# Optimization experiments

Hardware: AMD Instinct MI355X
Metric: run time of the kernel (lower is better)

## Reference

```python
import jax, jax.numpy as jnp
from jax import lax
import numpy as np

H, W = 240, 304
IN_CH, OUT_CH, K = 16, 32, 3
B = 8
N_PER = 65536
N = B * N_PER
CIN = IN_CH + 2  # pos + neg + features


def setup_inputs() -> dict:
    key = jax.random.key(0)
    k1, k2, k3, k4, k5 = jax.random.split(key, 5)
    # events columns: x, y, t in [0,1); polarity in {0,1}
    xyt = jax.random.uniform(k1, (N, 3), dtype=jnp.float32)
    pol = jax.random.randint(k2, (N, 1), 0, 2).astype(jnp.float32)
    events = jnp.concatenate([xyt, pol], axis=1)
    features = jax.random.normal(k3, (N, IN_CH), dtype=jnp.float32)
    offsets = (jnp.arange(1, B + 1, dtype=jnp.int64) * N_PER)  # cumulative counts
    # SubmanifoldConvolution params: one [CIN, OUT_CH] matrix per filter offset -> HWIO
    fan_in = K * K * CIN
    weight = jax.random.normal(k4, (K, K, CIN, OUT_CH), dtype=jnp.float32) / np.sqrt(fan_in)
    bias = jax.random.normal(k5, (OUT_CH,), dtype=jnp.float32) * 0.01
    return {"events": events, "features": features, "weight": weight,
            "bias": bias, "offsets": offsets}


def reference(events, features, weight, bias, offsets):
    n = events.shape[0]
    b = offsets.shape[0]
    # offset2batch: row i belongs to first sample whose cumulative offset exceeds i
    batch = jnp.searchsorted(offsets, jnp.arange(n, dtype=offsets.dtype), side="right").astype(jnp.int32)
    pos = events[:, 3:4]
    neg = 1.0 - pos
    sparse = jnp.concatenate([pos, neg, features], axis=1)  # [N, CIN]
    # yx = events[:, [1, 0]] scaled by (h, w), rounded to grid coords
    yi = jnp.clip(jnp.round(events[:, 1] * H).astype(jnp.int32), 0, H - 1)
    xi = jnp.clip(jnp.round(events[:, 0] * W).astype(jnp.int32), 0, W - 1)
    key = (batch * H + yi) * W + xi  # linear site id, [N]
    nseg = b * H * W
    # scn InputLayer mode=4: average features of duplicate coordinates
    feat_sum = jax.ops.segment_sum(sparse, key, num_segments=nseg)  # [nseg, CIN]
    cnt = jax.ops.segment_sum(jnp.ones((n,), sparse.dtype), key, num_segments=nseg)
    dense = feat_sum / jnp.maximum(cnt, 1.0)[:, None]
    dense = dense.reshape(b, H, W, CIN)  # zeros at inactive sites
    # Submanifold 3x3 conv: inactive neighbors are zero, so a dense SAME conv
    # evaluated only at active sites matches the submanifold rulebook math.
    out = lax.conv_general_dilated(dense, weight, window_strides=(1, 1),
                                   padding="SAME",
                                   dimension_numbers=("NHWC", "HWIO", "NHWC"))
    out = out.reshape(nseg, OUT_CH)
    # OutputLayer: read back per input row (active sites only), add bias there
    f = out[key] + bias  # [N, OUT_CH]
    return f
```

## Files before the change

### kernel.cpp

```cpp
#include <hip/hip_runtime.h>

#define Hh 240
#define Ww 304
#define IN_CH 16
#define OUT_CH 32
#define Bb 8
#define N_PER 65536
#define N_EV (Bb * N_PER)
#define CIN (IN_CH + 2)
#define NSEG (Bb * Hh * Ww)
#define NBLK 570

#define TW 32
#define TH 8
#define HW_ 34
#define HH_ 10
#define HALO_PIX (HH_ * HW_)
#define NXT_TILES 10
#define NYT_TILES 30
#define OPITCH 33

typedef __attribute__((ext_vector_type(8))) short bf16x8;
typedef __attribute__((ext_vector_type(4))) float f32x4;

__device__ __forceinline__ unsigned short f2bf(float x) {
  unsigned u = __float_as_uint(x);
  unsigned r = u + 0x7fffu + ((u >> 16) & 1u);
  return (unsigned short)(r >> 16);
}
__device__ __forceinline__ float bf2f(unsigned short b) {
  return __uint_as_float(((unsigned)b) << 16);
}
__device__ __forceinline__ unsigned pk2(float a, float b) {
  return (unsigned)f2bf(a) | ((unsigned)f2bf(b) << 16);
}

__global__ __launch_bounds__(256) void hist_rank_kernel(
    const float* __restrict__ events, const int* __restrict__ offsets,
    int* __restrict__ hist, int2* __restrict__ kr) {
  int i = blockIdx.x * blockDim.x + threadIdx.x;
  float4 ev = ((const float4*)events)[i];
  int yi = (int)rintf(ev.y * (float)Hh);
  yi = min(max(yi, 0), Hh - 1);
  int xi = (int)rintf(ev.x * (float)Ww);
  xi = min(max(xi, 0), Ww - 1);
  int b = 0;
#pragma unroll
  for (int j = 0; j < Bb; j++) b += (offsets[j] <= i) ? 1 : 0;
  int key = (b * Hh + yi) * Ww + xi;
  int pol = (ev.w != 0.0f) ? 1 : 0;
  int rank = atomicAdd(&hist[key], 1);
  kr[i] = make_int2(key | (pol << 31), rank);
}

__global__ __launch_bounds__(256) void scan1_kernel(
    const int* __restrict__ hist, int* __restrict__ baseLocal,
    int* __restrict__ blockSum) {
  __shared__ int lds[256];
  int b = blockIdx.x, t = threadIdx.x;
  int idx = b * 1024 + t * 4;
  int4 v = *(const int4*)(hist + idx);
  int s0 = v.x, s1 = s0 + v.y, s2 = s1 + v.z, s3 = s2 + v.w;
  lds[t] = s3;
  __syncthreads();
  int val = s3;
  for (int off = 1; off < 256; off <<= 1) {
    int n = (t >= off) ? lds[t - off] : 0;
    __syncthreads();
    val += n;
    lds[t] = val;
    __syncthreads();
  }
  int excl = val - s3;
  int4 o;
  o.x = excl; o.y = excl + s0; o.z = excl + s1; o.w = excl + s2;
  *(int4*)(baseLocal + idx) = o;
  if (t == 255) blockSum[b] = val;
}

__global__ __launch_bounds__(1024) void scan2_weights_kernel(
    const int* __restrict__ blockSum, int* __restrict__ blockOffset,
    const float* __restrict__ weight, unsigned short* __restrict__ wprep) {
  int t = threadIdx.x;
  if (blockIdx.x == 1) {
#pragma unroll
    for (int it = 0; it < 6; it++) {
      int idx = it * 1024 + t;
      int ky = idx >> 11;
      int rem = idx & 2047;
      int n = rem >> 6;
      int kl = rem & 63;
      unsigned short v = 0;
      if (kl < 54) {
        int kx = kl / 18, ci = kl - kx * 18;
        v = f2bf(weight[((ky * 3 + kx) * CIN + ci) * OUT_CH + n]);
      }
      wprep[idx] = v;
    }
    return;
  }
  __shared__ int lds[1024];
  int v = (t < NBLK) ? blockSum[t] : 0;
  lds[t] = v;
  __syncthreads();
  int val = v;
  for (int off = 1; off < 1024; off <<= 1) {
    int n = (t >= off) ? lds[t - off] : 0;
    __syncthreads();
    val += n;
    lds[t] = val;
    __syncthreads();
  }
  if (t < NBLK) blockOffset[t] = val - v;
  if (t == 0) blockOffset[NBLK] = lds[1023];
}

__global__ __launch_bounds__(256) void scatter_rec_kernel(
    const float* __restrict__ features, const int2* __restrict__ kr,
    const int* __restrict__ baseLocal, const int* __restrict__ blockOffset,
    uint4* __restrict__ sortedRec, int* __restrict__ sortedMeta) {
  int i = blockIdx.x * blockDim.x + threadIdx.x;
  int2 m = kr[i];
  int key = m.x & 0x7fffffff;
  int pos = baseLocal[key] + blockOffset[key >> 10] + m.y;
  const float4* f = (const float4*)(features + (size_t)i * IN_CH);
  float4 f0 = f[0], f1 = f[1], f2 = f[2], f3 = f[3];
  unsigned meta = (unsigned)i | ((unsigned)m.x & 0x80000000u);
  uint4* R = sortedRec + (size_t)pos * 3;
  R[0] = make_uint4(meta, pk2(f0.x, f0.y), pk2(f0.z, f0.w), pk2(f1.x, f1.y));
  R[1] = make_uint4(pk2(f1.z, f1.w), pk2(f2.x, f2.y), pk2(f2.z, f2.w),
                    pk2(f3.x, f3.y));
  R[2] = make_uint4(pk2(f3.z, f3.w), 0, 0, 0);
  sortedMeta[pos] = (int)meta;
}

__device__ __forceinline__ void accum_pixel(unsigned* smem,
                                            const uint4* __restrict__ sortedRec,
                                            int h, int base, int c) {
  float acc[CIN];
#pragma unroll
  for (int k = 0; k < CIN; k++) acc[k] = 0.0f;
  for (int j = 0; j < c; j++) {
    const uint4* R = sortedRec + (size_t)(base + j) * 3;
    uint4 r0 = R[0], r1 = R[1];
    unsigned d8 = ((const unsigned*)R)[8];
    float pol = (float)(r0.x >> 31);
    acc[0] += pol;
    acc[1] += 1.0f - pol;
    acc[2]  += bf2f((unsigned short)r0.y);  acc[3]  += bf2f((unsigned short)(r0.y >> 16));
    acc[4]  += bf2f((unsigned short)r0.z);  acc[5]  += bf2f((unsigned short)(r0.z >> 16));
    acc[6]  += bf2f((unsigned short)r0.w);  acc[7]  += bf2f((unsigned short)(r0.w >> 16));
    acc[8]  += bf2f((unsigned short)r1.x);  acc[9]  += bf2f((unsigned short)(r1.x >> 16));
    acc[10] += bf2f((unsigned short)r1.y);  acc[11] += bf2f((unsigned short)(r1.y >> 16));
    acc[12] += bf2f((unsigned short)r1.z);  acc[13] += bf2f((unsigned short)(r1.z >> 16));
    acc[14] += bf2f((unsigned short)r1.w);  acc[15] += bf2f((unsigned short)(r1.w >> 16));
    acc[16] += bf2f((unsigned short)d8);    acc[17] += bf2f((unsigned short)(d8 >> 16));
  }
  float inv = 1.0f / fmaxf((float)c, 1.0f);
  unsigned* row = smem + 9 * h;
#pragma unroll
  for (int k = 0; k < 9; k++) row[k] = pk2(acc[2 * k] * inv, acc[2 * k + 1] * inv);
}

__global__ __launch_bounds__(256) void fused_conv_kernel(
    const uint4* __restrict__ sortedRec, const int* __restrict__ sortedMeta,
    const int* __restrict__ baseLocal, const int* __restrict__ blockOffset,
    const unsigned short* __restrict__ wprep, const float* __restrict__ bias,
    float* __restrict__ out) {
  __shared__ unsigned smem[128 * OPITCH];
  __shared__ int ibase[TH * TW];
  __shared__ int icnt[TH * TW];

  int blk = blockIdx.x;
  int xt = blk % NXT_TILES;
  int rem = blk / NXT_TILES;
  int yt = rem % NYT_TILES;
  int b = rem / NYT_TILES;
  int x0 = xt * TW, y0 = yt * TH;
  int tid = threadIdx.x;

  if (tid < 12) smem[3060 + tid] = 0;

  int hA = tid, hB = tid + 256;
  bool hasB = hB < HALO_PIX;
  int baseA = 0, cA = 0, baseB = 0, cB = 0;
  {
    int hy = hA / HW_, hx = hA % HW_;
    int gy = y0 - 1 + hy, gx = x0 - 1 + hx;
    if (gy >= 0 && gy < Hh && gx >= 0 && gx < Ww) {
      int p = (b * Hh + gy) * Ww + gx;
      int bo = blockOffset[p >> 10];
      baseA = baseLocal[p] + bo;
      int nxt = ((p & 1023) != 1023) ? (baseLocal[p + 1] + bo)
                                     : blockOffset[(p >> 10) + 1];
      cA = nxt - baseA;
    }
  }
  if (hasB) {
    int hy = hB / HW_, hx = hB % HW_;
    int gy = y0 - 1 + hy, gx = x0 - 1 + hx;
    if (gy >= 0 && gy < Hh && gx >= 0 && gx < Ww) {
      int p = (b * Hh + gy) * Ww + gx;
      int bo = blockOffset[p >> 10];
      baseB = baseLocal[p] + bo;
      int nxt = ((p & 1023) != 1023) ? (baseLocal[p + 1] + bo)
                                     : blockOffset[(p >> 10) + 1];
      cB = nxt - baseB;
    }
  }
  accum_pixel(smem, sortedRec, hA, baseA, cA);
  if (hasB) accum_pixel(smem, sortedRec, hB, baseB, cB);
  {
    int hy = hA / HW_, hx = hA % HW_;
    if (hx >= 1 && hx <= TW && hy >= 1 && hy <= TH) {
      int t = (hy - 1) * TW + (hx - 1);
      ibase[t] = baseA;
      icnt[t] = cA;
    }
  }
  if (hasB) {
    int hy = hB / HW_, hx = hB % HW_;
    if (hx >= 1 && hx <= TW && hy >= 1 && hy <= TH) {
      int t = (hy - 1) * TW + (hx - 1);
      ibase[t] = baseB;
      icnt[t] = cB;
    }
  }
  __syncthreads();

  int wv = tid >> 6, lane = tid & 63;
  int quad = lane >> 4, lrow = lane & 15;

  f32x4 accf[4][2];
#pragma unroll
  for (int i = 0; i < 4; i++)
#pragma unroll
    for (int nt = 0; nt < 2; nt++) accf[i][nt] = (f32x4){0.f, 0.f, 0.f, 0.f};

  const unsigned* hp = smem;
#pragma unroll
  for (int ky = 0; ky < 3; ky++) {
    bf16x8 bfr[2][2];
#pragma unroll
    for (int kh = 0; kh < 2; kh++)
#pragma unroll
      for (int nt = 0; nt < 2; nt++) {
        int n = nt * 16 + lrow;
        bfr[kh][nt] = *(const bf16x8*)(wprep + ((ky * 32 + n) << 6) +
                                       kh * 32 + quad * 8);
      }
#pragma unroll
    for (int i = 0; i < 4; i++) {
      int t0 = (wv * 4 + i) * 16;
      int ox = (t0 & 31) + lrow;
      int oy = t0 >> 5;
      int idx0 = ((oy + ky) * HW_ + ox) * CIN;
#pragma unroll
      for (int kh = 0; kh < 2; kh++) {
        union { bf16x8 v; unsigned u[4]; } a;
        int ui = (idx0 >> 1) + kh * 16 + quad * 4;
        a.u[0] = hp[ui]; a.u[1] = hp[ui + 1];
        a.u[2] = hp[ui + 2]; a.u[3] = hp[ui + 3];
        accf[i][0] = __builtin_amdgcn_mfma_f32_16x16x32_bf16(
            a.v, bfr[kh][0], accf[i][0], 0, 0, 0);
        accf[i][1] = __builtin_amdgcn_mfma_f32_16x16x32_bf16(
            a.v, bfr[kh][1], accf[i][1], 0, 0, 0);
      }
    }
  }
  __syncthreads();

  float* outsh = (float*)smem;
  float bn0 = bias[lrow], bn1 = bias[16 + lrow];
  int gx = x0 + (tid & 31);
  int c = icnt[tid];
  int base = ibase[tid];
#pragma unroll
  for (int ch = 0; ch < 2; ch++) {
#pragma unroll
    for (int ii = 0; ii < 2; ii++) {
      int i = ch * 2 + ii;
      int lidx = ii * 16 + quad * 4;
      int row = wv * 32 + lidx;
#pragma unroll
      for (int r = 0; r < 4; r++) {
        outsh[(row + r) * OPITCH + lrow] = accf[i][0][r] + bn0;
        outsh[(row + r) * OPITCH + 16 + lrow] = accf[i][1][r] + bn1;
      }
    }
    __syncthreads();
    if (((tid >> 5) & 1) == ch && gx < Ww && c > 0) {
      int row = (tid >> 6) * 32 + ((tid & 63) - ch * 32);
      const float* rp = outsh + row * OPITCH;
      float4 o0 = make_float4(rp[0], rp[1], rp[2], rp[3]);
      float4 o1 = make_float4(rp[4], rp[5], rp[6], rp[7]);
      float4 o2 = make_float4(rp[8], rp[9], rp[10], rp[11]);
      float4 o3 = make_float4(rp[12], rp[13], rp[14], rp[15]);
      float4 o4 = make_float4(rp[16], rp[17], rp[18], rp[19]);
      float4 o5 = make_float4(rp[20], rp[21], rp[22], rp[23]);
      float4 o6 = make_float4(rp[24], rp[25], rp[26], rp[27]);
      float4 o7 = make_float4(rp[28], rp[29], rp[30], rp[31]);
      for (int j = 0; j < c; j++) {
        int ev = sortedMeta[base + j] & 0x7fffffff;
        float4* op = (float4*)(out + (size_t)ev * OUT_CH);
        op[0] = o0; op[1] = o1; op[2] = o2; op[3] = o3;
        op[4] = o4; op[5] = o5; op[6] = o6; op[7] = o7;
      }
    }
    __syncthreads();
  }
}

extern "C" void kernel_launch(void* const* d_in, const int* in_sizes, int n_in,
                              void* d_out, int out_size, void* d_ws,
                              size_t ws_size, hipStream_t stream) {
  const float* events = (const float*)d_in[0];
  const float* features = (const float*)d_in[1];
  const float* weight = (const float*)d_in[2];
  const float* bias = (const float*)d_in[3];
  const int* offsets = (const int*)d_in[4];
  float* out = (float*)d_out;

  uint4* sortedRec = (uint4*)d_ws;
  int* sortedMeta = (int*)(sortedRec + (size_t)N_EV * 3);
  int2* kr = (int2*)(sortedMeta + N_EV);
  int* hist = (int*)(kr + N_EV);
  int* baseLocal = hist + NSEG;
  int* blockOffset = baseLocal + NSEG;
  int* blockSum = blockOffset + 1024;
  unsigned short* wprep = (unsigned short*)(blockSum + 1024);

  hipMemsetAsync(hist, 0, (size_t)NSEG * sizeof(int), stream);

  hist_rank_kernel<<<N_EV / 256, 256, 0, stream>>>(events, offsets, hist, kr);
  scan1_kernel<<<NBLK, 256, 0, stream>>>(hist, baseLocal, blockSum);
  scan2_weights_kernel<<<2, 1024, 0, stream>>>(blockSum, blockOffset, weight,
                                               wprep);
  scatter_rec_kernel<<<N_EV / 256, 256, 0, stream>>>(
      features, kr, baseLocal, blockOffset, sortedRec, sortedMeta);
  fused_conv_kernel<<<Bb * NYT_TILES * NXT_TILES, 256, 0, stream>>>(
      sortedRec, sortedMeta, baseLocal, blockOffset, wprep, bias, out);
}
```

Baseline: 194.9 us.

## Split per-pixel averaging into separate densify kernel with padded dense grid

Per-pixel averaging of duplicate events moves out of the conv kernel into a new densify kernel. It writes a padded bf16 dense grid (10 dwords per pixel), which the conv kernel loads as a halo tile. This stops each conv block from recomputing the halo pixels it shares with neighbouring tiles. Polarity is now stored as pre-packed bf16 in 64-byte records, the scan runs in place, and the weight layout is repadded to a 20-channel stride. The cost is an extra launch plus a write and read of the full dense grid, which is roughly 23 MB.

```diff
diff --git a/kernel.cpp b/kernel.cpp
--- a/kernel.cpp
+++ b/kernel.cpp
@@ -11,14 +11,17 @@
 #define NSEG (Bb * Hh * Ww)
 #define NBLK 570
 
+#define DP 10
+
 #define TW 32
 #define TH 8
 #define HW_ 34
 #define HH_ 10
-#define HALO_PIX (HH_ * HW_)
 #define NXT_TILES 10
 #define NYT_TILES 30
 #define OPITCH 33
+#define HALO_DW (HH_ * HW_ * DP)
+#define HALO_LD 3424
 
 typedef __attribute__((ext_vector_type(8))) short bf16x8;
 typedef __attribute__((ext_vector_type(4))) float f32x4;
@@ -53,13 +56,12 @@
   kr[i] = make_int2(key | (pol << 31), rank);
 }
 
-__global__ __launch_bounds__(256) void scan1_kernel(
-    const int* __restrict__ hist, int* __restrict__ baseLocal,
-    int* __restrict__ blockSum) {
+__global__ __launch_bounds__(256) void scan1_kernel(int* __restrict__ data,
+                                                    int* __restrict__ blockSum) {
   __shared__ int lds[256];
   int b = blockIdx.x, t = threadIdx.x;
   int idx = b * 1024 + t * 4;
-  int4 v = *(const int4*)(hist + idx);
+  int4 v = *(const int4*)(data + idx);
   int s0 = v.x, s1 = s0 + v.y, s2 = s1 + v.z, s3 = s2 + v.w;
   lds[t] = s3;
   __syncthreads();
@@ -74,7 +76,7 @@
   int excl = val - s3;
   int4 o;
   o.x = excl; o.y = excl + s0; o.z = excl + s1; o.w = excl + s2;
-  *(int4*)(baseLocal + idx) = o;
+  *(int4*)(data + idx) = o;
   if (t == 255) blockSum[b] = val;
 }
 
@@ -91,9 +93,9 @@
       int n = rem >> 6;
       int kl = rem & 63;
       unsigned short v = 0;
-      if (kl < 54) {
-        int kx = kl / 18, ci = kl - kx * 18;
-        v = f2bf(weight[((ky * 3 + kx) * CIN + ci) * OUT_CH + n]);
+      if (kl < 60) {
+        int kx = kl / 20, ci = kl - kx * 20;
+        if (ci < 18) v = f2bf(weight[((ky * 3 + kx) * CIN + ci) * OUT_CH + n]);
       }
       wprep[idx] = v;
     }
@@ -123,30 +125,36 @@
   int2 m = kr[i];
   int key = m.x & 0x7fffffff;
   int pos = baseLocal[key] + blockOffset[key >> 10] + m.y;
+  float pol = (float)(((unsigned)m.x) >> 31);
   const float4* f = (const float4*)(features + (size_t)i * IN_CH);
   float4 f0 = f[0], f1 = f[1], f2 = f[2], f3 = f[3];
-  unsigned meta = (unsigned)i | ((unsigned)m.x & 0x80000000u);
-  uint4* R = sortedRec + (size_t)pos * 3;
-  R[0] = make_uint4(meta, pk2(f0.x, f0.y), pk2(f0.z, f0.w), pk2(f1.x, f1.y));
+  uint4* R = sortedRec + (size_t)pos * 4;
+  R[0] = make_uint4(pk2(pol, 1.0f - pol), pk2(f0.x, f0.y), pk2(f0.z, f0.w),
+                    pk2(f1.x, f1.y));
   R[1] = make_uint4(pk2(f1.z, f1.w), pk2(f2.x, f2.y), pk2(f2.z, f2.w),
                     pk2(f3.x, f3.y));
   R[2] = make_uint4(pk2(f3.z, f3.w), 0, 0, 0);
-  sortedMeta[pos] = (int)meta;
-}
-
-__device__ __forceinline__ void accum_pixel(unsigned* smem,
-                                            const uint4* __restrict__ sortedRec,
-                                            int h, int base, int c) {
+  R[3] = make_uint4(0, 0, 0, 0);
+  sortedMeta[pos] = i;
+}
+
+__global__ __launch_bounds__(256) void densify_kernel(
+    const uint4* __restrict__ sortedRec, const int* __restrict__ baseLocal,
+    const int* __restrict__ blockOffset, unsigned* __restrict__ dense) {
+  int p = blockIdx.x * 256 + threadIdx.x;
+  int bo = blockOffset[p >> 10];
+  int base = baseLocal[p] + bo;
+  int nxt = ((p & 1023) != 1023) ? (baseLocal[p + 1] + bo)
+                                 : blockOffset[(p >> 10) + 1];
+  int c = nxt - base;
   float acc[CIN];
 #pragma unroll
   for (int k = 0; k < CIN; k++) acc[k] = 0.0f;
   for (int j = 0; j < c; j++) {
-    const uint4* R = sortedRec + (size_t)(base + j) * 3;
+    const uint4* R = sortedRec + (size_t)(base + j) * 4;
     uint4 r0 = R[0], r1 = R[1];
     unsigned d8 = ((const unsigned*)R)[8];
-    float pol = (float)(r0.x >> 31);
-    acc[0] += pol;
-    acc[1] += 1.0f - pol;
+    acc[0]  += bf2f((unsigned short)r0.x);  acc[1]  += bf2f((unsigned short)(r0.x >> 16));
     acc[2]  += bf2f((unsigned short)r0.y);  acc[3]  += bf2f((unsigned short)(r0.y >> 16));
     acc[4]  += bf2f((unsigned short)r0.z);  acc[5]  += bf2f((unsigned short)(r0.z >> 16));
     acc[6]  += bf2f((unsigned short)r0.w);  acc[7]  += bf2f((unsigned short)(r0.w >> 16));
@@ -157,19 +165,18 @@
     acc[16] += bf2f((unsigned short)d8);    acc[17] += bf2f((unsigned short)(d8 >> 16));
   }
   float inv = 1.0f / fmaxf((float)c, 1.0f);
-  unsigned* row = smem + 9 * h;
-#pragma unroll
-  for (int k = 0; k < 9; k++) row[k] = pk2(acc[2 * k] * inv, acc[2 * k + 1] * inv);
+  unsigned* dp = dense + (size_t)p * DP;
+#pragma unroll
+  for (int k = 0; k < 9; k++) dp[k] = pk2(acc[2 * k] * inv, acc[2 * k + 1] * inv);
+  dp[9] = 0;
 }
 
 __global__ __launch_bounds__(256) void fused_conv_kernel(
-    const uint4* __restrict__ sortedRec, const int* __restrict__ sortedMeta,
+    const unsigned* __restrict__ dense, const int* __restrict__ sortedMeta,
     const int* __restrict__ baseLocal, const int* __restrict__ blockOffset,
     const unsigned short* __restrict__ wprep, const float* __restrict__ bias,
     float* __restrict__ out) {
   __shared__ unsigned smem[128 * OPITCH];
-  __shared__ int ibase[TH * TW];
-  __shared__ int icnt[TH * TW];
 
   int blk = blockIdx.x;
   int xt = blk % NXT_TILES;
@@ -179,52 +186,29 @@
   int x0 = xt * TW, y0 = yt * TH;
   int tid = threadIdx.x;
 
-  if (tid < 12) smem[3060 + tid] = 0;
-
-  int hA = tid, hB = tid + 256;
-  bool hasB = hB < HALO_PIX;
-  int baseA = 0, cA = 0, baseB = 0, cB = 0;
-  {
-    int hy = hA / HW_, hx = hA % HW_;
-    int gy = y0 - 1 + hy, gx = x0 - 1 + hx;
-    if (gy >= 0 && gy < Hh && gx >= 0 && gx < Ww) {
-      int p = (b * Hh + gy) * Ww + gx;
-      int bo = blockOffset[p >> 10];
-      baseA = baseLocal[p] + bo;
-      int nxt = ((p & 1023) != 1023) ? (baseLocal[p + 1] + bo)
-                                     : blockOffset[(p >> 10) + 1];
-      cA = nxt - baseA;
-    }
-  }
-  if (hasB) {
-    int hy = hB / HW_, hx = hB % HW_;
-    int gy = y0 - 1 + hy, gx = x0 - 1 + hx;
-    if (gy >= 0 && gy < Hh && gx >= 0 && gx < Ww) {
-      int p = (b * Hh + gy) * Ww + gx;
-      int bo = blockOffset[p >> 10];
-      baseB = baseLocal[p] + bo;
-      int nxt = ((p & 1023) != 1023) ? (baseLocal[p + 1] + bo)
-                                     : blockOffset[(p >> 10) + 1];
-      cB = nxt - baseB;
-    }
-  }
-  accum_pixel(smem, sortedRec, hA, baseA, cA);
-  if (hasB) accum_pixel(smem, sortedRec, hB, baseB, cB);
-  {
-    int hy = hA / HW_, hx = hA % HW_;
-    if (hx >= 1 && hx <= TW && hy >= 1 && hy <= TH) {
-      int t = (hy - 1) * TW + (hx - 1);
-      ibase[t] = baseA;
-      icnt[t] = cA;
-    }
-  }
-  if (hasB) {
-    int hy = hB / HW_, hx = hB % HW_;
-    if (hx >= 1 && hx <= TW && hy >= 1 && hy <= TH) {
-      int t = (hy - 1) * TW + (hx - 1);
-      ibase[t] = baseB;
-      icnt[t] = cB;
-    }
+  int tx = tid & 31, ty = tid >> 5;
+  int gxo = x0 + tx;
+  int c = 0, base = 0;
+  if (gxo < Ww) {
+    int p = (b * Hh + y0 + ty) * Ww + gxo;
+    int bo = blockOffset[p >> 10];
+    base = baseLocal[p] + bo;
+    int nxt = ((p & 1023) != 1023) ? (baseLocal[p + 1] + bo)
+                                   : blockOffset[(p >> 10) + 1];
+    c = nxt - base;
+  }
+  int m0 = (c > 0) ? sortedMeta[base] : 0;
+
+  for (int i = tid; i < HALO_LD; i += 256) {
+    int r = i / 340;
+    int cd = i - r * 340;
+    int hx = cd / 10;
+    int k = cd - hx * 10;
+    int gy = y0 - 1 + r, gx = x0 - 1 + hx;
+    unsigned v = 0;
+    if (gy >= 0 && gy < Hh && gx >= 0 && gx < Ww)
+      v = dense[(size_t)((b * Hh + gy) * Ww + gx) * DP + k];
+    smem[i] = v;
   }
   __syncthreads();
 
@@ -254,11 +238,11 @@
       int t0 = (wv * 4 + i) * 16;
       int ox = (t0 & 31) + lrow;
       int oy = t0 >> 5;
-      int idx0 = ((oy + ky) * HW_ + ox) * CIN;
+      int pix = (oy + ky) * HW_ + ox;
 #pragma unroll
       for (int kh = 0; kh < 2; kh++) {
         union { bf16x8 v; unsigned u[4]; } a;
-        int ui = (idx0 >> 1) + kh * 16 + quad * 4;
+        int ui = pix * DP + kh * 16 + quad * 4;
         a.u[0] = hp[ui]; a.u[1] = hp[ui + 1];
         a.u[2] = hp[ui + 2]; a.u[3] = hp[ui + 3];
         accf[i][0] = __builtin_amdgcn_mfma_f32_16x16x32_bf16(
@@ -272,9 +256,6 @@
 
   float* outsh = (float*)smem;
   float bn0 = bias[lrow], bn1 = bias[16 + lrow];
-  int gx = x0 + (tid & 31);
-  int c = icnt[tid];
-  int base = ibase[tid];
 #pragma unroll
   for (int ch = 0; ch < 2; ch++) {
 #pragma unroll
@@ -289,7 +270,7 @@
       }
     }
     __syncthreads();
-    if (((tid >> 5) & 1) == ch && gx < Ww && c > 0) {
+    if (((tid >> 5) & 1) == ch && gxo < Ww && c > 0) {
       int row = (tid >> 6) * 32 + ((tid & 63) - ch * 32);
       const float* rp = outsh + row * OPITCH;
       float4 o0 = make_float4(rp[0], rp[1], rp[2], rp[3]);
@@ -301,7 +282,7 @@
       float4 o6 = make_float4(rp[24], rp[25], rp[26], rp[27]);
       float4 o7 = make_float4(rp[28], rp[29], rp[30], rp[31]);
       for (int j = 0; j < c; j++) {
-        int ev = sortedMeta[base + j] & 0x7fffffff;
+        int ev = (j == 0) ? m0 : sortedMeta[base + j];
         float4* op = (float4*)(out + (size_t)ev * OUT_CH);
         op[0] = o0; op[1] = o1; op[2] = o2; op[3] = o3;
         op[4] = o4; op[5] = o5; op[6] = o6; op[7] = o7;
@@ -322,22 +303,24 @@
   float* out = (float*)d_out;
 
   uint4* sortedRec = (uint4*)d_ws;
-  int* sortedMeta = (int*)(sortedRec + (size_t)N_EV * 3);
+  unsigned* dense = (unsigned*)(sortedRec + (size_t)N_EV * 4);
+  int* sortedMeta = (int*)(dense + (size_t)NSEG * DP);
   int2* kr = (int2*)(sortedMeta + N_EV);
   int* hist = (int*)(kr + N_EV);
-  int* baseLocal = hist + NSEG;
-  int* blockOffset = baseLocal + NSEG;
+  int* blockOffset = hist + NSEG;
   int* blockSum = blockOffset + 1024;
   unsigned short* wprep = (unsigned short*)(blockSum + 1024);
 
   hipMemsetAsync(hist, 0, (size_t)NSEG * sizeof(int), stream);
 
   hist_rank_kernel<<<N_EV / 256, 256, 0, stream>>>(events, offsets, hist, kr);
-  scan1_kernel<<<NBLK, 256, 0, stream>>>(hist, baseLocal, blockSum);
+  scan1_kernel<<<NBLK, 256, 0, stream>>>(hist, blockSum);
   scan2_weights_kernel<<<2, 1024, 0, stream>>>(blockSum, blockOffset, weight,
                                                wprep);
   scatter_rec_kernel<<<N_EV / 256, 256, 0, stream>>>(
-      features, kr, baseLocal, blockOffset, sortedRec, sortedMeta);
+      features, kr, hist, blockOffset, sortedRec, sortedMeta);
+  densify_kernel<<<NSEG / 256, 256, 0, stream>>>(sortedRec, hist, blockOffset,
+                                                 dense);
   fused_conv_kernel<<<Bb * NYT_TILES * NXT_TILES, 256, 0, stream>>>(
-      sortedRec, sortedMeta, baseLocal, blockOffset, wprep, bias, out);
-}
+      dense, sortedMeta, hist, blockOffset, wprep, bias, out);
+}
```

Result: slower. 206.2 us (+5.8%).
